# Optimization experiments

Measured on AMD Instinct MI355X. Metric: run time of the kernel, lower is better.

The kernel has to match this reference:

```python
import jax, jax.numpy as jnp
import numpy as np
from functools import partial

DIM = 128      # LSTM hidden size
NODES = 81     # graph nodes
T = 12         # sequence length


def _lstm_layer(x, Wih, Whh, bih, bhh):
    """PyTorch-style LSTM layer. x: (N, T, in) -> (N, T, H). Gate order i,f,g,o."""
    N = x.shape[0]
    H = Whh.shape[1]
    b = bih + bhh

    def step(carry, xt):
        h, c = carry
        gates = xt @ Wih.T + h @ Whh.T + b              # (N, 4H)
        i, f, g, o = jnp.split(gates, 4, axis=-1)
        i = jax.nn.sigmoid(i)
        f = jax.nn.sigmoid(f)
        g = jnp.tanh(g)
        o = jax.nn.sigmoid(o)
        c = f * c + i * g
        h = o * jnp.tanh(c)
        return (h, c), h

    h0 = jnp.zeros((N, H), x.dtype)
    c0 = jnp.zeros((N, H), x.dtype)
    xT = jnp.swapaxes(x, 0, 1)                           # (T, N, in)
    _, hs = jax.lax.scan(step, (h0, c0), xT)
    return jnp.swapaxes(hs, 0, 1)                        # (N, T, H)


def setup_inputs() -> dict:
    key = jax.random.key(0)
    ks = jax.random.split(key, 16)
    k = 1.0 / np.sqrt(DIM)
    u = lambda kk, shape: jax.random.uniform(kk, shape, jnp.float32, -k, k)
    inp = {
        "g_data": jax.random.normal(ks[0], (512, T, NODES), jnp.float32),
        "weights": jax.random.normal(ks[1], (NODES, NODES), jnp.float32) * 0.1,
        # LSTM layer 0 (input size 1)
        "Wih0": u(ks[2], (4 * DIM, 1)),
        "Whh0": u(ks[3], (4 * DIM, DIM)),
        "bih0": u(ks[4], (4 * DIM,)),
        "bhh0": u(ks[5], (4 * DIM,)),
        # LSTM layer 1 (input size DIM)
        "Wih1": u(ks[6], (4 * DIM, DIM)),
        "Whh1": u(ks[7], (4 * DIM, DIM)),
        "bih1": u(ks[8], (4 * DIM,)),
        "bhh1": u(ks[9], (4 * DIM,)),
        # MLP head 128 -> 32 -> 1
        "fc1_w": u(ks[10], (32, DIM)),
        "fc1_b": u(ks[11], (32,)),
        "fc2_w": u(ks[12], (1, 32)),
        "fc2_b": u(ks[13], (1,)),
    }
    return inp


def reference(g_data, weights, Wih0, Whh0, bih0, bhh0, Wih1, Whh1, bih1, bhh1,
              fc1_w, fc1_b, fc2_w, fc2_b):
    B = g_data.shape[0]
    # Vectorized graph aggregation: income[:, :, i] = g_data @ weights[:, i]
    income = jnp.einsum('bta,an->bnt', g_data, weights)   # (B, 81, 12)
    x = income.reshape(B * NODES, T, 1)                   # one scalar seq per (sample, node)
    h1 = _lstm_layer(x, Wih0, Whh0, bih0, bhh0)           # (B*81, 12, 128)
    h2 = _lstm_layer(h1, Wih1, Whh1, bih1, bhh1)          # (B*81, 12, 128)
    last = h2[:, -1, :]                                   # only last step feeds the output
    hid = jax.nn.relu(last @ fc1_w.T + fc1_b)             # (B*81, 32)
    out = jax.nn.relu(hid @ fc2_w.T + fc2_b)              # (B*81, 1)
    return out.reshape(B, NODES).reshape(B, 1, NODES, 1)
```

## Files before the change

### kernel.cpp

```cpp
#include <hip/hip_runtime.h>
#include <math.h>

#define NODES 81
#define T_STEPS 12
#define NSEQ 41472
#define HID 128
#define SEQB 32

typedef unsigned short ushort;
typedef unsigned int uint;
typedef __attribute__((ext_vector_type(8))) _Float16 half8;
typedef __attribute__((ext_vector_type(4))) float f32x4;

#define MFMA(A, B, C) __builtin_amdgcn_mfma_f32_16x16x32_f16((A), (B), (C), 0, 0, 0)

__device__ __forceinline__ float sigf(float v) {
    return __builtin_amdgcn_rcpf(1.f + __builtin_amdgcn_exp2f(v * -1.442695041f));
}
__device__ __forceinline__ float tanhf_(float v) {
    return fmaf(2.f, __builtin_amdgcn_rcpf(1.f + __builtin_amdgcn_exp2f(v * -2.885390082f)), -1.f);
}

__global__ void prep_kernel(const float* __restrict__ Whh0,
                            const float* __restrict__ Wih1,
                            const float* __restrict__ Whh1,
                            const float* __restrict__ Wih0,
                            const float* __restrict__ bih0, const float* __restrict__ bhh0,
                            const float* __restrict__ bih1, const float* __restrict__ bhh1,
                            _Float16* __restrict__ WF0,
                            _Float16* __restrict__ WF1i,
                            _Float16* __restrict__ WF1h,
                            float* __restrict__ wq,
                            float* __restrict__ b0q,
                            float* __restrict__ b1q)
{
    int idx = blockIdx.x * 256 + threadIdx.x;
    if (idx < 196608) {
        int mat = idx >> 16;
        int li  = idx & 65535;
        int j   = li & 7;
        int l   = (li >> 3) & 63;
        int nt  = (li >> 9) & 31;
        int ks  = li >> 14;
        int k = ks * 32 + (l >> 4) * 8 + j;
        int n = nt * 16 + (l & 15);
        const float* W = (mat == 0) ? Whh0 : (mat == 1 ? Wih1 : Whh1);
        _Float16* D = (mat == 0) ? WF0 : (mat == 1 ? WF1i : WF1h);
        D[li] = (_Float16)W[n * 128 + k];
    } else if (idx < 197120) {
        int jp = idx - 196608;
        int u = jp >> 2, t4 = jp & 3;
        wq[jp] = Wih0[t4 * 128 + u];
    } else if (idx < 197632) {
        int jp = idx - 197120;
        int u = jp >> 2, t4 = jp & 3;
        b0q[jp] = bih0[t4 * 128 + u] + bhh0[t4 * 128 + u];
    } else if (idx < 198144) {
        int jp = idx - 197632;
        int u = jp >> 2, t4 = jp & 3;
        b1q[jp] = bih1[t4 * 128 + u] + bhh1[t4 * 128 + u];
    }
}

__global__ void income_kernel(const float* __restrict__ g_data,
                              const float* __restrict__ w,
                              float* __restrict__ x)
{
    int idx = blockIdx.x * 256 + threadIdx.x;
    int n = idx % NODES;
    int r = idx / NODES;
    int t = r % T_STEPS;
    int b = r / T_STEPS;
    const float* grow = g_data + (b * T_STEPS + t) * NODES;
    float s = 0.f;
    #pragma unroll 3
    for (int a = 0; a < NODES; ++a)
        s += grow[a] * w[a * NODES + n];
    x[t * NSEQ + b * NODES + n] = s;
}

__global__ __launch_bounds__(512, 1) void lstm_main(
    const float* __restrict__ x,
    const _Float16* __restrict__ WF0,
    const _Float16* __restrict__ WF1i,
    const _Float16* __restrict__ WF1h,
    const float* __restrict__ wq,
    const float* __restrict__ b0q,
    const float* __restrict__ b1q,
    const float* __restrict__ fc1_w,
    const float* __restrict__ fc1_b,
    const float* __restrict__ fc2_w,
    const float* __restrict__ fc2_b,
    float* __restrict__ out)
{
    __shared__ __align__(16) _Float16 hA0[8192];
    __shared__ __align__(16) _Float16 hA1[8192];

    const int tid = threadIdx.x;
    const int l   = tid & 63;
    const int gr  = tid >> 6;
    const int l15 = l & 15;
    const int l16 = l >> 4;
    const int u   = gr * 16 + l15;
    const int seq0 = blockIdx.x * SEQB;

    for (int i = tid; i < 4096; i += 512) {
        ((uint*)hA0)[i] = 0u; ((uint*)hA1)[i] = 0u;
    }

    const _Float16* wfb0 = WF0  + gr * 512 + l * 8;
    const _Float16* wfb1 = WF1i + gr * 512 + l * 8;
    const _Float16* wfb2 = WF1h + gr * 512 + l * 8;

    float c0[8], c1[8];
    #pragma unroll
    for (int i = 0; i < 8; ++i) { c0[i] = 0.f; c1[i] = 0.f; }
    __syncthreads();

    int cur = 0;
    for (int t = 0; t < T_STEPS; ++t) {
        const int nxt = cur ^ 1;
        const float* xb = x + t * NSEQ + seq0;
        f32x4 acc[2][4];

        #pragma unroll
        for (int mt = 0; mt < 2; ++mt)
            #pragma unroll
            for (int t4 = 0; t4 < 4; ++t4) acc[mt][t4] = (f32x4){0.f, 0.f, 0.f, 0.f};
        #pragma unroll 1
        for (int ks = 0; ks < 4; ++ks) {
            const int ao = cur * 4096 + (ks * 4 + l16) * 256 + l15 * 8;
            half8 a0 = *(const half8*)(hA0 + ao);
            half8 a1 = *(const half8*)(hA0 + ao + 128);
            #pragma unroll
            for (int t4 = 0; t4 < 4; ++t4) {
                half8 b = *(const half8*)(wfb0 + ks * 16384 + t4 * 4096);
                acc[0][t4] = MFMA(a0, b, acc[0][t4]);
                acc[1][t4] = MFMA(a1, b, acc[1][t4]);
            }
        }
        {
            float4 wv  = *(const float4*)(wq  + u * 4);
            float4 bv0 = *(const float4*)(b0q + u * 4);
            #pragma unroll
            for (int mt = 0; mt < 2; ++mt) {
                #pragma unroll
                for (int r = 0; r < 4; ++r) {
                    int m = mt * 16 + l16 * 4 + r;
                    float xv = xb[m];
                    float gi = acc[mt][0][r] + xv * wv.x + bv0.x;
                    float gf = acc[mt][1][r] + xv * wv.y + bv0.y;
                    float gg = acc[mt][2][r] + xv * wv.z + bv0.z;
                    float go = acc[mt][3][r] + xv * wv.w + bv0.w;
                    float iv = sigf(gi), fv = sigf(gf), gv = tanhf_(gg), ov = sigf(go);
                    float c = fv * c0[mt * 4 + r] + iv * gv;
                    c0[mt * 4 + r] = c;
                    float h = ov * tanhf_(c);
                    hA0[nxt * 4096 + (u >> 3) * 256 + m * 8 + (u & 7)] = (_Float16)h;
                }
            }
        }
        __syncthreads();

        #pragma unroll
        for (int mt = 0; mt < 2; ++mt)
            #pragma unroll
            for (int t4 = 0; t4 < 4; ++t4) acc[mt][t4] = (f32x4){0.f, 0.f, 0.f, 0.f};
        #pragma unroll 1
        for (int ks = 0; ks < 4; ++ks) {
            const int a0o = nxt * 4096 + (ks * 4 + l16) * 256 + l15 * 8;
            half8 a0 = *(const half8*)(hA0 + a0o);
            half8 a1 = *(const half8*)(hA0 + a0o + 128);
            #pragma unroll
            for (int t4 = 0; t4 < 4; ++t4) {
                half8 b = *(const half8*)(wfb1 + ks * 16384 + t4 * 4096);
                acc[0][t4] = MFMA(a0, b, acc[0][t4]);
                acc[1][t4] = MFMA(a1, b, acc[1][t4]);
            }
        }
        #pragma unroll 1
        for (int ks = 0; ks < 4; ++ks) {
            const int a1o = cur * 4096 + (ks * 4 + l16) * 256 + l15 * 8;
            half8 a0 = *(const half8*)(hA1 + a1o);
            half8 a1 = *(const half8*)(hA1 + a1o + 128);
            #pragma unroll
            for (int t4 = 0; t4 < 4; ++t4) {
                half8 b = *(const half8*)(wfb2 + ks * 16384 + t4 * 4096);
                acc[0][t4] = MFMA(a0, b, acc[0][t4]);
                acc[1][t4] = MFMA(a1, b, acc[1][t4]);
            }
        }
        {
            float4 bv1 = *(const float4*)(b1q + u * 4);
            #pragma unroll
            for (int mt = 0; mt < 2; ++mt) {
                #pragma unroll
                for (int r = 0; r < 4; ++r) {
                    int m = mt * 16 + l16 * 4 + r;
                    float gi = acc[mt][0][r] + bv1.x;
                    float gf = acc[mt][1][r] + bv1.y;
                    float gg = acc[mt][2][r] + bv1.z;
                    float go = acc[mt][3][r] + bv1.w;
                    float iv = sigf(gi), fv = sigf(gf), gv = tanhf_(gg), ov = sigf(go);
                    float c = fv * c1[mt * 4 + r] + iv * gv;
                    c1[mt * 4 + r] = c;
                    float h = ov * tanhf_(c);
                    hA1[nxt * 4096 + (u >> 3) * 256 + m * 8 + (u & 7)] = (_Float16)h;
                }
            }
        }
        __syncthreads();
        cur = nxt;
    }

    float* hidb = (float*)hA0;
    float hv[2];
    #pragma unroll
    for (int r2 = 0; r2 < 2; ++r2) {
        int task = tid + r2 * 512;
        int s = task >> 5, j = task & 31;
        float sum = fc1_b[j];
        const float* wrow = fc1_w + j * HID;
        #pragma unroll 4
        for (int kq = 0; kq < 16; ++kq) {
            half8 H = *(const half8*)(hA1 + cur * 4096 + kq * 256 + s * 8);
            #pragma unroll
            for (int j8 = 0; j8 < 8; ++j8)
                sum += (float)H[j8] * wrow[kq * 8 + j8];
        }
        hv[r2] = fmaxf(sum, 0.f);
    }
    __syncthreads();
    #pragma unroll
    for (int r2 = 0; r2 < 2; ++r2) {
        int task = tid + r2 * 512;
        hidb[(task >> 5) * 33 + (task & 31)] = hv[r2];
    }
    __syncthreads();
    if (tid < SEQB) {
        float sum = fc2_b[0];
        #pragma unroll
        for (int j = 0; j < 32; ++j) sum += hidb[tid * 33 + j] * fc2_w[j];
        out[seq0 + tid] = fmaxf(sum, 0.f);
    }
}

extern "C" void kernel_launch(void* const* d_in, const int* in_sizes, int n_in,
                              void* d_out, int out_size, void* d_ws, size_t ws_size,
                              hipStream_t stream)
{
    const float* g_data = (const float*)d_in[0];
    const float* weights = (const float*)d_in[1];
    const float* Wih0   = (const float*)d_in[2];
    const float* Whh0   = (const float*)d_in[3];
    const float* bih0   = (const float*)d_in[4];
    const float* bhh0   = (const float*)d_in[5];
    const float* Wih1   = (const float*)d_in[6];
    const float* Whh1   = (const float*)d_in[7];
    const float* bih1   = (const float*)d_in[8];
    const float* bhh1   = (const float*)d_in[9];
    const float* fc1_w  = (const float*)d_in[10];
    const float* fc1_b  = (const float*)d_in[11];
    const float* fc2_w  = (const float*)d_in[12];
    const float* fc2_b  = (const float*)d_in[13];
    float* out = (float*)d_out;

    float* ws = (float*)d_ws;
    float*     x    = ws;
    _Float16*  WF0  = (_Float16*)(x + NSEQ * T_STEPS);
    _Float16*  WF1i = WF0 + 65536;
    _Float16*  WF1h = WF1i + 65536;
    float*     wqp  = (float*)(WF1h + 65536);
    float*     b0q  = wqp + 512;
    float*     b1q  = b0q + 512;

    prep_kernel<<<774, 256, 0, stream>>>(Whh0, Wih1, Whh1, Wih0, bih0, bhh0, bih1, bhh1,
                                         WF0, WF1i, WF1h, wqp, b0q, b1q);
    income_kernel<<<1944, 256, 0, stream>>>(g_data, weights, x);
    lstm_main<<<NSEQ / SEQB, 512, 0, stream>>>(x, WF0, WF1i, WF1h, wqp, b0q, b1q,
                                               fc1_w, fc1_b, fc2_w, fc2_b, out);
}
```

Baseline: 438.7 us.

## Halve sequences per block and keep LSTM weight fragments resident in registers

```diff
diff --git a/kernel.cpp b/kernel.cpp
--- a/kernel.cpp
+++ b/kernel.cpp
@@ -5,7 +5,7 @@
 #define T_STEPS 12
 #define NSEQ 41472
 #define HID 128
-#define SEQB 32
+#define SEQB 16
 
 typedef unsigned short ushort;
 typedef unsigned int uint;
@@ -93,8 +93,8 @@
     const float* __restrict__ fc2_b,
     float* __restrict__ out)
 {
-    __shared__ __align__(16) _Float16 hA0[8192];
-    __shared__ __align__(16) _Float16 hA1[8192];
+    __shared__ __align__(16) _Float16 hA0[4096];
+    __shared__ __align__(16) _Float16 hA1[4096];
 
     const int tid = threadIdx.x;
     const int l   = tid & 63;
@@ -104,137 +104,108 @@
     const int u   = gr * 16 + l15;
     const int seq0 = blockIdx.x * SEQB;
 
-    for (int i = tid; i < 4096; i += 512) {
+    for (int i = tid; i < 2048; i += 512) {
         ((uint*)hA0)[i] = 0u; ((uint*)hA1)[i] = 0u;
     }
 
     const _Float16* wfb0 = WF0  + gr * 512 + l * 8;
     const _Float16* wfb1 = WF1i + gr * 512 + l * 8;
     const _Float16* wfb2 = WF1h + gr * 512 + l * 8;
-
-    float c0[8], c1[8];
+    half8 B0[4][4], B1[4][4], B2[4][4];
     #pragma unroll
-    for (int i = 0; i < 8; ++i) { c0[i] = 0.f; c1[i] = 0.f; }
+    for (int ks = 0; ks < 4; ++ks)
+        #pragma unroll
+        for (int t4 = 0; t4 < 4; ++t4) {
+            B0[ks][t4] = *(const half8*)(wfb0 + ks * 16384 + t4 * 4096);
+            B1[ks][t4] = *(const half8*)(wfb1 + ks * 16384 + t4 * 4096);
+            B2[ks][t4] = *(const half8*)(wfb2 + ks * 16384 + t4 * 4096);
+        }
+
+    const float4 wv  = *(const float4*)(wq  + u * 4);
+    const float4 bv0 = *(const float4*)(b0q + u * 4);
+    const float4 bv1 = *(const float4*)(b1q + u * 4);
+
+    float c0[4], c1[4];
+    #pragma unroll
+    for (int i = 0; i < 4; ++i) { c0[i] = 0.f; c1[i] = 0.f; }
     __syncthreads();
+
+    const int wrbase = (u >> 3) * 128 + (u & 7);
 
     int cur = 0;
     for (int t = 0; t < T_STEPS; ++t) {
         const int nxt = cur ^ 1;
-        const float* xb = x + t * NSEQ + seq0;
-        f32x4 acc[2][4];
-
-        #pragma unroll
-        for (int mt = 0; mt < 2; ++mt)
-            #pragma unroll
-            for (int t4 = 0; t4 < 4; ++t4) acc[mt][t4] = (f32x4){0.f, 0.f, 0.f, 0.f};
-        #pragma unroll 1
+        const float4 xv4 = *(const float4*)(x + t * NSEQ + seq0 + l16 * 4);
+
+        f32x4 acc[4];
+
+        #pragma unroll
+        for (int t4 = 0; t4 < 4; ++t4) acc[t4] = (f32x4){0.f, 0.f, 0.f, 0.f};
+        #pragma unroll
         for (int ks = 0; ks < 4; ++ks) {
-            const int ao = cur * 4096 + (ks * 4 + l16) * 256 + l15 * 8;
-            half8 a0 = *(const half8*)(hA0 + ao);
-            half8 a1 = *(const half8*)(hA0 + ao + 128);
-            #pragma unroll
-            for (int t4 = 0; t4 < 4; ++t4) {
-                half8 b = *(const half8*)(wfb0 + ks * 16384 + t4 * 4096);
-                acc[0][t4] = MFMA(a0, b, acc[0][t4]);
-                acc[1][t4] = MFMA(a1, b, acc[1][t4]);
-            }
-        }
-        {
-            float4 wv  = *(const float4*)(wq  + u * 4);
-            float4 bv0 = *(const float4*)(b0q + u * 4);
-            #pragma unroll
-            for (int mt = 0; mt < 2; ++mt) {
-                #pragma unroll
-                for (int r = 0; r < 4; ++r) {
-                    int m = mt * 16 + l16 * 4 + r;
-                    float xv = xb[m];
-                    float gi = acc[mt][0][r] + xv * wv.x + bv0.x;
-                    float gf = acc[mt][1][r] + xv * wv.y + bv0.y;
-                    float gg = acc[mt][2][r] + xv * wv.z + bv0.z;
-                    float go = acc[mt][3][r] + xv * wv.w + bv0.w;
-                    float iv = sigf(gi), fv = sigf(gf), gv = tanhf_(gg), ov = sigf(go);
-                    float c = fv * c0[mt * 4 + r] + iv * gv;
-                    c0[mt * 4 + r] = c;
-                    float h = ov * tanhf_(c);
-                    hA0[nxt * 4096 + (u >> 3) * 256 + m * 8 + (u & 7)] = (_Float16)h;
-                }
-            }
+            half8 a = *(const half8*)(hA0 + cur * 2048 + (ks * 4 + l16) * 128 + l15 * 8);
+            #pragma unroll
+            for (int t4 = 0; t4 < 4; ++t4) acc[t4] = MFMA(a, B0[ks][t4], acc[t4]);
+        }
+        #pragma unroll
+        for (int r = 0; r < 4; ++r) {
+            int m = l16 * 4 + r;
+            float gi = acc[0][r] + xv4[r] * wv.x + bv0.x;
+            float gf = acc[1][r] + xv4[r] * wv.y + bv0.y;
+            float gg = acc[2][r] + xv4[r] * wv.z + bv0.z;
+            float go = acc[3][r] + xv4[r] * wv.w + bv0.w;
+            float iv = sigf(gi), fv = sigf(gf), gv = tanhf_(gg), ov = sigf(go);
+            float c = fv * c0[r] + iv * gv;
+            c0[r] = c;
+            hA0[nxt * 2048 + wrbase + m * 8] = (_Float16)(ov * tanhf_(c));
         }
         __syncthreads();
 
         #pragma unroll
-        for (int mt = 0; mt < 2; ++mt)
-            #pragma unroll
-            for (int t4 = 0; t4 < 4; ++t4) acc[mt][t4] = (f32x4){0.f, 0.f, 0.f, 0.f};
-        #pragma unroll 1
+        for (int t4 = 0; t4 < 4; ++t4) acc[t4] = (f32x4){0.f, 0.f, 0.f, 0.f};
+        #pragma unroll
         for (int ks = 0; ks < 4; ++ks) {
-            const int a0o = nxt * 4096 + (ks * 4 + l16) * 256 + l15 * 8;
-            half8 a0 = *(const half8*)(hA0 + a0o);
-            half8 a1 = *(const half8*)(hA0 + a0o + 128);
-            #pragma unroll
-            for (int t4 = 0; t4 < 4; ++t4) {
-                half8 b = *(const half8*)(wfb1 + ks * 16384 + t4 * 4096);
-                acc[0][t4] = MFMA(a0, b, acc[0][t4]);
-                acc[1][t4] = MFMA(a1, b, acc[1][t4]);
-            }
-        }
-        #pragma unroll 1
+            half8 a = *(const half8*)(hA0 + nxt * 2048 + (ks * 4 + l16) * 128 + l15 * 8);
+            #pragma unroll
+            for (int t4 = 0; t4 < 4; ++t4) acc[t4] = MFMA(a, B1[ks][t4], acc[t4]);
+        }
+        #pragma unroll
         for (int ks = 0; ks < 4; ++ks) {
-            const int a1o = cur * 4096 + (ks * 4 + l16) * 256 + l15 * 8;
-            half8 a0 = *(const half8*)(hA1 + a1o);
-            half8 a1 = *(const half8*)(hA1 + a1o + 128);
-            #pragma unroll
-            for (int t4 = 0; t4 < 4; ++t4) {
-                half8 b = *(const half8*)(wfb2 + ks * 16384 + t4 * 4096);
-                acc[0][t4] = MFMA(a0, b, acc[0][t4]);
-                acc[1][t4] = MFMA(a1, b, acc[1][t4]);
-            }
-        }
-        {
-            float4 bv1 = *(const float4*)(b1q + u * 4);
-            #pragma unroll
-            for (int mt = 0; mt < 2; ++mt) {
-                #pragma unroll
-                for (int r = 0; r < 4; ++r) {
-                    int m = mt * 16 + l16 * 4 + r;
-                    float gi = acc[mt][0][r] + bv1.x;
-                    float gf = acc[mt][1][r] + bv1.y;
-                    float gg = acc[mt][2][r] + bv1.z;
-                    float go = acc[mt][3][r] + bv1.w;
-                    float iv = sigf(gi), fv = sigf(gf), gv = tanhf_(gg), ov = sigf(go);
-                    float c = fv * c1[mt * 4 + r] + iv * gv;
-                    c1[mt * 4 + r] = c;
-                    float h = ov * tanhf_(c);
-                    hA1[nxt * 4096 + (u >> 3) * 256 + m * 8 + (u & 7)] = (_Float16)h;
-                }
-            }
-        }
-        __syncthreads();
+            half8 a = *(const half8*)(hA1 + cur * 2048 + (ks * 4 + l16) * 128 + l15 * 8);
+            #pragma unroll
+            for (int t4 = 0; t4 < 4; ++t4) acc[t4] = MFMA(a, B2[ks][t4], acc[t4]);
+        }
+        #pragma unroll
+        for (int r = 0; r < 4; ++r) {
+            int m = l16 * 4 + r;
+            float gi = acc[0][r] + bv1.x;
+            float gf = acc[1][r] + bv1.y;
+            float gg = acc[2][r] + bv1.z;
+            float go = acc[3][r] + bv1.w;
+            float iv = sigf(gi), fv = sigf(gf), gv = tanhf_(gg), ov = sigf(go);
+            float c = fv * c1[r] + iv * gv;
+            c1[r] = c;
+            hA1[nxt * 2048 + wrbase + m * 8] = (_Float16)(ov * tanhf_(c));
+        }
         cur = nxt;
     }
+    __syncthreads();
 
     float* hidb = (float*)hA0;
-    float hv[2];
-    #pragma unroll
-    for (int r2 = 0; r2 < 2; ++r2) {
-        int task = tid + r2 * 512;
-        int s = task >> 5, j = task & 31;
+    {
+        int s = tid >> 5, j = tid & 31;
         float sum = fc1_b[j];
         const float* wrow = fc1_w + j * HID;
         #pragma unroll 4
         for (int kq = 0; kq < 16; ++kq) {
-            half8 H = *(const half8*)(hA1 + cur * 4096 + kq * 256 + s * 8);
+            half8 H = *(const half8*)(hA1 + cur * 2048 + kq * 128 + s * 8);
             #pragma unroll
             for (int j8 = 0; j8 < 8; ++j8)
                 sum += (float)H[j8] * wrow[kq * 8 + j8];
         }
-        hv[r2] = fmaxf(sum, 0.f);
-    }
-    __syncthreads();
-    #pragma unroll
-    for (int r2 = 0; r2 < 2; ++r2) {
-        int task = tid + r2 * 512;
-        hidb[(task >> 5) * 33 + (task & 31)] = hv[r2];
+        float hv = fmaxf(sum, 0.f);
+        __syncthreads();
+        hidb[s * 33 + j] = hv;
     }
     __syncthreads();
     if (tid < SEQB) {
```

Result: faster. 383.6 us, median of 2 (-12.6%).
